# Performance work log

Hardware: AMD Instinct MI355X
Metric: run time of the kernel (lower is better)

Reference implementation:

```python
import jax, jax.numpy as jnp
import numpy as np


def setup_inputs() -> dict:
    key = jax.random.key(0)
    tensor = jax.random.normal(key, (4096, 3072), dtype=jnp.float32)
    return {"tensor": tensor}


def reference(tensor) -> jnp.ndarray:
    # Original: full_products[i,j] = mean_d((x_i * x_j)^2), zero diagonal, sum.
    # Identity: mean_d((x_i*x_j)^2) = (1/D) * sum_d (x_i^2)_d (x_j^2)_d = (Y Y^T / D)[i,j] with Y = x^2.
    B = tensor.shape[0]
    Y = jnp.square(tensor.reshape(B, -1))  # [B, D]
    D = Y.shape[1]
    G = jnp.matmul(Y, Y.T) / D  # [B, B] Gram of squared features
    # sum over off-diagonal entries == total sum minus trace
    return jnp.sum(G) - jnp.trace(G)
```

## Files before the change

kernel.cpp:

```cpp
#include <hip/hip_runtime.h>


typedef float f4 __attribute__((ext_vector_type(4)));

#define NROWS 4096
#define NCOLS 3072
#define NC4     768
#define GBX     24
#define NCHUNK  64
#define NBLK1   (GBX * NCHUNK)
#define TPB     256
#define DINV (1.0 / (double)NCOLS)

#define WS_CS_OFF  0
#define WS_COL_OFF 128
#define WS_Q_OFF   (WS_COL_OFF + NCHUNK * NCOLS * 4)
#define WS_CNT_OFF (WS_Q_OFF + NBLK1 * 4)

__global__ __launch_bounds__(TPB) void k1_colsq(const float* __restrict__ x,
                                                float* __restrict__ col_part,
                                                float* __restrict__ q_part,
                                                unsigned int* __restrict__ counter) {
    const int t    = threadIdx.x;
    const int tc   = t & 31;
    const int rsub = t >> 5;
    const int c4   = blockIdx.x * 32 + tc;
    const int r0   = blockIdx.y * 64 + rsub * 8;
    const f4* __restrict__ xv = (const f4*)x;

    if (t == 0 && blockIdx.x == 0 && blockIdx.y == 0) *counter = 0u;

    f4 s = (f4)(0.f);
    float q = 0.f;
    #pragma unroll
    for (int i = 0; i < 8; ++i) {
        f4 v = __builtin_nontemporal_load(&xv[(size_t)(r0 + i) * NC4 + c4]);
        f4 sq = v * v;
        s += sq;
        q = fmaf(sq.x, sq.x, q); q = fmaf(sq.y, sq.y, q);
        q = fmaf(sq.z, sq.z, q); q = fmaf(sq.w, sq.w, q);
    }

    __shared__ f4    part[7][32];
    __shared__ float qs[4];
    if (rsub) part[rsub - 1][tc] = s;
    #pragma unroll
    for (int off = 32; off; off >>= 1) q += __shfl_down(q, off);
    if ((t & 63) == 0) qs[t >> 6] = q;
    __syncthreads();

    if (rsub == 0) {
        f4 p = ((part[0][tc] + part[1][tc]) + (part[2][tc] + part[3][tc]))
             + ((part[4][tc] + part[5][tc]) + (part[6][tc] + s));
        ((f4*)col_part)[(size_t)blockIdx.y * NC4 + c4] = p;
    }
    if (t == 0)
        q_part[blockIdx.y * GBX + blockIdx.x] = (qs[0] + qs[1]) + (qs[2] + qs[3]);
}

__global__ __launch_bounds__(TPB) void k2_finish(const float* __restrict__ col_part,
                                                 const float* __restrict__ q_part,
                                                 double* __restrict__ cs_part,
                                                 unsigned int* __restrict__ counter,
                                                 float* __restrict__ out) {
    const int t = threadIdx.x;
    const int b = blockIdx.x;
    const int tc = t & 63, rsub = t >> 6;
    __shared__ f4 part[3][64];
    __shared__ double dsh[4];
    double partial = 0.0;

    if (b < 12) {
        const f4* __restrict__ cp4 = (const f4*)col_part;
        const int c4 = b * 64 + tc;
        f4 s = (f4)(0.f);
        #pragma unroll
        for (int i = 0; i < 16; ++i)
            s += cp4[(size_t)(rsub * 16 + i) * NC4 + c4];
        if (rsub) part[rsub - 1][tc] = s;
        __syncthreads();
        if (rsub == 0) {
            f4 p0 = part[0][tc], p1 = part[1][tc], p2 = part[2][tc];
            double cx = ((double)s.x + (double)p0.x) + ((double)p1.x + (double)p2.x);
            double cy = ((double)s.y + (double)p0.y) + ((double)p1.y + (double)p2.y);
            double cz = ((double)s.z + (double)p0.z) + ((double)p1.z + (double)p2.z);
            double cw = ((double)s.w + (double)p0.w) + ((double)p1.w + (double)p2.w);
            partial = (cx * cx + cy * cy) + (cz * cz + cw * cw);
            #pragma unroll
            for (int off = 32; off; off >>= 1) partial += __shfl_down(partial, off);
        }
    } else {
        double qd = 0.0;
        #pragma unroll
        for (int i = 0; i < 6; ++i) qd += (double)q_part[t + i * TPB];
        #pragma unroll
        for (int off = 32; off; off >>= 1) qd += __shfl_down(qd, off);
        if ((t & 63) == 0) dsh[rsub] = qd;
        __syncthreads();
        if (t == 0) partial = (dsh[0] + dsh[1]) + (dsh[2] + dsh[3]);
    }

    if (t == 0) {
        __hip_atomic_store(&cs_part[b], partial, __ATOMIC_RELEASE, __HIP_MEMORY_SCOPE_AGENT);
        unsigned int old = __hip_atomic_fetch_add(counter, 1u, __ATOMIC_ACQ_REL,
                                                  __HIP_MEMORY_SCOPE_AGENT);
        if (old == 12u) {
            double acc = 0.0;
            #pragma unroll
            for (int i = 0; i < 12; ++i)
                acc += __hip_atomic_load(&cs_part[i], __ATOMIC_ACQUIRE,
                                         __HIP_MEMORY_SCOPE_AGENT);
            acc -= __hip_atomic_load(&cs_part[12], __ATOMIC_ACQUIRE,
                                     __HIP_MEMORY_SCOPE_AGENT);
            out[0] = (float)(acc * DINV);
        }
    }
}

extern "C" void kernel_launch(void* const* d_in, const int* in_sizes, int n_in,
                              void* d_out, int out_size, void* d_ws, size_t ws_size,
                              hipStream_t stream) {
    const float* x = (const float*)d_in[0];
    float* out = (float*)d_out;
    char* ws = (char*)d_ws;
    double* cs_part  = (double*)(ws + WS_CS_OFF);
    float*  col_part = (float*)(ws + WS_COL_OFF);
    float*  q_part   = (float*)(ws + WS_Q_OFF);
    unsigned int* counter = (unsigned int*)(ws + WS_CNT_OFF);

    k1_colsq<<<dim3(GBX, NCHUNK), TPB, 0, stream>>>(x, col_part, q_part, counter);
    k2_finish<<<13, TPB, 0, stream>>>(col_part, q_part, cs_part, counter, out);
}
```

Measured before the change: 17.24 us.

## Restructure column-square reduction into full-row blocks with larger second-stage partials

The first kernel now runs 256 blocks of 768 threads, each covering 16 full rows, and writes its column partial sums straight out with no shared-memory combine. The second kernel then reduces 256 partial rows instead of 64, spread over 24 stripes plus one block for the squared-norm term. This removes the in-block LDS reduction in stage one and uses contiguous full-row reads. In exchange the intermediate buffer grows fourfold (about 3 MB) and stage two has to read more data.

```diff
diff --git a/kernel.cpp b/kernel.cpp
--- a/kernel.cpp
+++ b/kernel.cpp
@@ -6,96 +6,89 @@
 #define NROWS 4096
 #define NCOLS 3072
 #define NC4     768
-#define GBX     24
-#define NCHUNK  64
-#define NBLK1   (GBX * NCHUNK)
-#define TPB     256
+#define TPB1    768
+#define RPB     16
+#define NBLK1   (NROWS / RPB)
+#define NSTRIPE 24
+#define TPB2    256
 #define DINV (1.0 / (double)NCOLS)
 
 #define WS_CS_OFF  0
-#define WS_COL_OFF 128
-#define WS_Q_OFF   (WS_COL_OFF + NCHUNK * NCOLS * 4)
+#define WS_COL_OFF 256
+#define WS_Q_OFF   (WS_COL_OFF + NBLK1 * NCOLS * 4)
 #define WS_CNT_OFF (WS_Q_OFF + NBLK1 * 4)
 
-__global__ __launch_bounds__(TPB) void k1_colsq(const float* __restrict__ x,
-                                                float* __restrict__ col_part,
-                                                float* __restrict__ q_part,
-                                                unsigned int* __restrict__ counter) {
-    const int t    = threadIdx.x;
-    const int tc   = t & 31;
-    const int rsub = t >> 5;
-    const int c4   = blockIdx.x * 32 + tc;
-    const int r0   = blockIdx.y * 64 + rsub * 8;
+__global__ __launch_bounds__(TPB1) void k1_colsq(const float* __restrict__ x,
+                                                 float* __restrict__ col_part,
+                                                 float* __restrict__ q_part,
+                                                 unsigned int* __restrict__ counter) {
+    const int t = threadIdx.x;
+    const int b = blockIdx.x;
     const f4* __restrict__ xv = (const f4*)x;
+    const size_t base = (size_t)b * RPB * NC4 + t;
 
-    if (t == 0 && blockIdx.x == 0 && blockIdx.y == 0) *counter = 0u;
+    if (t == 0 && b == 0) *counter = 0u;
 
     f4 s = (f4)(0.f);
     float q = 0.f;
     #pragma unroll
-    for (int i = 0; i < 8; ++i) {
-        f4 v = __builtin_nontemporal_load(&xv[(size_t)(r0 + i) * NC4 + c4]);
+    for (int r = 0; r < RPB; ++r) {
+        f4 v = __builtin_nontemporal_load(&xv[base + (size_t)r * NC4]);
         f4 sq = v * v;
         s += sq;
         q = fmaf(sq.x, sq.x, q); q = fmaf(sq.y, sq.y, q);
         q = fmaf(sq.z, sq.z, q); q = fmaf(sq.w, sq.w, q);
     }
+    ((f4*)col_part)[(size_t)b * NC4 + t] = s;
 
-    __shared__ f4    part[7][32];
-    __shared__ float qs[4];
-    if (rsub) part[rsub - 1][tc] = s;
     #pragma unroll
     for (int off = 32; off; off >>= 1) q += __shfl_down(q, off);
+    __shared__ float qs[12];
     if ((t & 63) == 0) qs[t >> 6] = q;
     __syncthreads();
-
-    if (rsub == 0) {
-        f4 p = ((part[0][tc] + part[1][tc]) + (part[2][tc] + part[3][tc]))
-             + ((part[4][tc] + part[5][tc]) + (part[6][tc] + s));
-        ((f4*)col_part)[(size_t)blockIdx.y * NC4 + c4] = p;
+    if (t == 0) {
+        float qq = ((qs[0] + qs[1]) + (qs[2] + qs[3]))
+                 + ((qs[4] + qs[5]) + (qs[6] + qs[7]))
+                 + ((qs[8] + qs[9]) + (qs[10] + qs[11]));
+        q_part[b] = qq;
     }
-    if (t == 0)
-        q_part[blockIdx.y * GBX + blockIdx.x] = (qs[0] + qs[1]) + (qs[2] + qs[3]);
 }
 
-__global__ __launch_bounds__(TPB) void k2_finish(const float* __restrict__ col_part,
-                                                 const float* __restrict__ q_part,
-                                                 double* __restrict__ cs_part,
-                                                 unsigned int* __restrict__ counter,
-                                                 float* __restrict__ out) {
+__global__ __launch_bounds__(TPB2) void k2_finish(const float* __restrict__ col_part,
+                                                  const float* __restrict__ q_part,
+                                                  double* __restrict__ cs_part,
+                                                  unsigned int* __restrict__ counter,
+                                                  float* __restrict__ out) {
     const int t = threadIdx.x;
     const int b = blockIdx.x;
-    const int tc = t & 63, rsub = t >> 6;
-    __shared__ f4 part[3][64];
+    const int tc = t & 31, rsub = t >> 5;
+    __shared__ f4 part[7][32];
     __shared__ double dsh[4];
     double partial = 0.0;
 
-    if (b < 12) {
+    if (b < NSTRIPE) {
         const f4* __restrict__ cp4 = (const f4*)col_part;
-        const int c4 = b * 64 + tc;
+        const int c4 = b * 32 + tc;
         f4 s = (f4)(0.f);
         #pragma unroll
-        for (int i = 0; i < 16; ++i)
-            s += cp4[(size_t)(rsub * 16 + i) * NC4 + c4];
+        for (int i = 0; i < 32; ++i)
+            s += cp4[(size_t)(rsub * 32 + i) * NC4 + c4];
         if (rsub) part[rsub - 1][tc] = s;
         __syncthreads();
         if (rsub == 0) {
-            f4 p0 = part[0][tc], p1 = part[1][tc], p2 = part[2][tc];
-            double cx = ((double)s.x + (double)p0.x) + ((double)p1.x + (double)p2.x);
-            double cy = ((double)s.y + (double)p0.y) + ((double)p1.y + (double)p2.y);
-            double cz = ((double)s.z + (double)p0.z) + ((double)p1.z + (double)p2.z);
-            double cw = ((double)s.w + (double)p0.w) + ((double)p1.w + (double)p2.w);
+            f4 tot = ((s + part[0][tc]) + (part[1][tc] + part[2][tc]))
+                   + ((part[3][tc] + part[4][tc]) + (part[5][tc] + part[6][tc]));
+            double cx = (double)tot.x, cy = (double)tot.y;
+            double cz = (double)tot.z, cw = (double)tot.w;
             partial = (cx * cx + cy * cy) + (cz * cz + cw * cw);
             #pragma unroll
-            for (int off = 32; off; off >>= 1) partial += __shfl_down(partial, off);
+            for (int off = 16; off; off >>= 1) partial += __shfl_down(partial, off);
         }
     } else {
-        double qd = 0.0;
-        #pragma unroll
-        for (int i = 0; i < 6; ++i) qd += (double)q_part[t + i * TPB];
+        double qd = (double)q_part[t];
         #pragma unroll
         for (int off = 32; off; off >>= 1) qd += __shfl_down(qd, off);
-        if ((t & 63) == 0) dsh[rsub] = qd;
+        if ((t & 63) == 0) dsh[t >> 6] = qd;
         __syncthreads();
         if (t == 0) partial = (dsh[0] + dsh[1]) + (dsh[2] + dsh[3]);
     }
@@ -104,13 +97,13 @@
         __hip_atomic_store(&cs_part[b], partial, __ATOMIC_RELEASE, __HIP_MEMORY_SCOPE_AGENT);
         unsigned int old = __hip_atomic_fetch_add(counter, 1u, __ATOMIC_ACQ_REL,
                                                   __HIP_MEMORY_SCOPE_AGENT);
-        if (old == 12u) {
+        if (old == NSTRIPE) {
             double acc = 0.0;
             #pragma unroll
-            for (int i = 0; i < 12; ++i)
+            for (int i = 0; i < NSTRIPE; ++i)
                 acc += __hip_atomic_load(&cs_part[i], __ATOMIC_ACQUIRE,
                                          __HIP_MEMORY_SCOPE_AGENT);
-            acc -= __hip_atomic_load(&cs_part[12], __ATOMIC_ACQUIRE,
+            acc -= __hip_atomic_load(&cs_part[NSTRIPE], __ATOMIC_ACQUIRE,
                                      __HIP_MEMORY_SCOPE_AGENT);
             out[0] = (float)(acc * DINV);
         }
@@ -128,6 +121,6 @@
     float*  q_part   = (float*)(ws + WS_Q_OFF);
     unsigned int* counter = (unsigned int*)(ws + WS_CNT_OFF);
 
-    k1_colsq<<<dim3(GBX, NCHUNK), TPB, 0, stream>>>(x, col_part, q_part, counter);
-    k2_finish<<<13, TPB, 0, stream>>>(col_part, q_part, cs_part, counter, out);
+    k1_colsq<<<NBLK1, TPB1, 0, stream>>>(x, col_part, q_part, counter);
+    k2_finish<<<NSTRIPE + 1, TPB2, 0, stream>>>(col_part, q_part, cs_part, counter, out);
 }
```

After: 20.68 us. 19.9% more time.

## Fuse column reduction and finish into one kernel with float atomics and last-block tail

Applied to the files above, without the earlier changes.

Replaces the two-kernel scheme (per-chunk column partials, then a finishing kernel) with a single kernel. Each block atomically adds its column sums into one shared array of 3072 floats, and the last block to arrive, found with a counter, computes the sum of squares and subtracts the diagonal term. A memset clears the accumulators before the launch. This removes the partial-sum round trip and one kernel launch, but adds a memset operation, contention on float atomics (64 blocks per cell), and summation order that is no longer deterministic.

```diff
diff --git a/kernel.cpp b/kernel.cpp
--- a/kernel.cpp
+++ b/kernel.cpp
@@ -12,23 +12,24 @@
 #define TPB     256
 #define DINV (1.0 / (double)NCOLS)
 
-#define WS_CS_OFF  0
-#define WS_COL_OFF 128
-#define WS_Q_OFF   (WS_COL_OFF + NCHUNK * NCOLS * 4)
-#define WS_CNT_OFF (WS_Q_OFF + NBLK1 * 4)
+#define WS_CELLS_OFF  0
+#define WS_CNT_OFF    (NCOLS * 4)
+#define WS_ZERO_BYTES (NCOLS * 4 + 4)
+#define WS_Q_OFF      (NCOLS * 4 + 128)
 
-__global__ __launch_bounds__(TPB) void k1_colsq(const float* __restrict__ x,
-                                                float* __restrict__ col_part,
-                                                float* __restrict__ q_part,
-                                                unsigned int* __restrict__ counter) {
+__global__ __launch_bounds__(TPB) void fused_orthreg(
+        const float* __restrict__ x,
+        float* __restrict__ cells,
+        float* __restrict__ q_part,
+        unsigned int* __restrict__ counter,
+        float* __restrict__ out) {
     const int t    = threadIdx.x;
     const int tc   = t & 31;
     const int rsub = t >> 5;
     const int c4   = blockIdx.x * 32 + tc;
     const int r0   = blockIdx.y * 64 + rsub * 8;
+    const int bid  = blockIdx.y * GBX + blockIdx.x;
     const f4* __restrict__ xv = (const f4*)x;
-
-    if (t == 0 && blockIdx.x == 0 && blockIdx.y == 0) *counter = 0u;
 
     f4 s = (f4)(0.f);
     float q = 0.f;
@@ -43,6 +44,7 @@
 
     __shared__ f4    part[7][32];
     __shared__ float qs[4];
+    __shared__ int   lastflag;
     if (rsub) part[rsub - 1][tc] = s;
     #pragma unroll
     for (int off = 32; off; off >>= 1) q += __shfl_down(q, off);
@@ -52,69 +54,43 @@
     if (rsub == 0) {
         f4 p = ((part[0][tc] + part[1][tc]) + (part[2][tc] + part[3][tc]))
              + ((part[4][tc] + part[5][tc]) + (part[6][tc] + s));
-        ((f4*)col_part)[(size_t)blockIdx.y * NC4 + c4] = p;
-    }
-    if (t == 0)
-        q_part[blockIdx.y * GBX + blockIdx.x] = (qs[0] + qs[1]) + (qs[2] + qs[3]);
-}
-
-__global__ __launch_bounds__(TPB) void k2_finish(const float* __restrict__ col_part,
-                                                 const float* __restrict__ q_part,
-                                                 double* __restrict__ cs_part,
-                                                 unsigned int* __restrict__ counter,
-                                                 float* __restrict__ out) {
-    const int t = threadIdx.x;
-    const int b = blockIdx.x;
-    const int tc = t & 63, rsub = t >> 6;
-    __shared__ f4 part[3][64];
-    __shared__ double dsh[4];
-    double partial = 0.0;
-
-    if (b < 12) {
-        const f4* __restrict__ cp4 = (const f4*)col_part;
-        const int c4 = b * 64 + tc;
-        f4 s = (f4)(0.f);
-        #pragma unroll
-        for (int i = 0; i < 16; ++i)
-            s += cp4[(size_t)(rsub * 16 + i) * NC4 + c4];
-        if (rsub) part[rsub - 1][tc] = s;
-        __syncthreads();
-        if (rsub == 0) {
-            f4 p0 = part[0][tc], p1 = part[1][tc], p2 = part[2][tc];
-            double cx = ((double)s.x + (double)p0.x) + ((double)p1.x + (double)p2.x);
-            double cy = ((double)s.y + (double)p0.y) + ((double)p1.y + (double)p2.y);
-            double cz = ((double)s.z + (double)p0.z) + ((double)p1.z + (double)p2.z);
-            double cw = ((double)s.w + (double)p0.w) + ((double)p1.w + (double)p2.w);
-            partial = (cx * cx + cy * cy) + (cz * cz + cw * cw);
-            #pragma unroll
-            for (int off = 32; off; off >>= 1) partial += __shfl_down(partial, off);
-        }
-    } else {
-        double qd = 0.0;
-        #pragma unroll
-        for (int i = 0; i < 6; ++i) qd += (double)q_part[t + i * TPB];
-        #pragma unroll
-        for (int off = 32; off; off >>= 1) qd += __shfl_down(qd, off);
-        if ((t & 63) == 0) dsh[rsub] = qd;
-        __syncthreads();
-        if (t == 0) partial = (dsh[0] + dsh[1]) + (dsh[2] + dsh[3]);
-    }
-
-    if (t == 0) {
-        __hip_atomic_store(&cs_part[b], partial, __ATOMIC_RELEASE, __HIP_MEMORY_SCOPE_AGENT);
-        unsigned int old = __hip_atomic_fetch_add(counter, 1u, __ATOMIC_ACQ_REL,
-                                                  __HIP_MEMORY_SCOPE_AGENT);
-        if (old == 12u) {
-            double acc = 0.0;
-            #pragma unroll
-            for (int i = 0; i < 12; ++i)
-                acc += __hip_atomic_load(&cs_part[i], __ATOMIC_ACQUIRE,
-                                         __HIP_MEMORY_SCOPE_AGENT);
-            acc -= __hip_atomic_load(&cs_part[12], __ATOMIC_ACQUIRE,
-                                     __HIP_MEMORY_SCOPE_AGENT);
-            out[0] = (float)(acc * DINV);
+        __hip_atomic_fetch_add(&cells[c4 * 4 + 0], p.x, __ATOMIC_RELAXED, __HIP_MEMORY_SCOPE_AGENT);
+        __hip_atomic_fetch_add(&cells[c4 * 4 + 1], p.y, __ATOMIC_RELAXED, __HIP_MEMORY_SCOPE_AGENT);
+        __hip_atomic_fetch_add(&cells[c4 * 4 + 2], p.z, __ATOMIC_RELAXED, __HIP_MEMORY_SCOPE_AGENT);
+        __hip_atomic_fetch_add(&cells[c4 * 4 + 3], p.w, __ATOMIC_RELAXED, __HIP_MEMORY_SCOPE_AGENT);
+        if (t == 0) {
+            float qq = (qs[0] + qs[1]) + (qs[2] + qs[3]);
+            __hip_atomic_store(&q_part[bid], qq, __ATOMIC_RELAXED, __HIP_MEMORY_SCOPE_AGENT);
+            asm volatile("s_waitcnt vmcnt(0)" ::: "memory");
+            unsigned int old = __hip_atomic_fetch_add(counter, 1u, __ATOMIC_RELAXED,
+                                                      __HIP_MEMORY_SCOPE_AGENT);
+            lastflag = (old == NBLK1 - 1);
         }
     }
+    __syncthreads();
+    if (!lastflag) return;
+
+    double acc = 0.0;
+    #pragma unroll
+    for (int i = 0; i < NCOLS / TPB; ++i) {
+        float cv = __hip_atomic_load(&cells[t + i * TPB], __ATOMIC_RELAXED,
+                                     __HIP_MEMORY_SCOPE_AGENT);
+        double cd = (double)cv;
+        acc += cd * cd;
+    }
+    double qa = 0.0;
+    #pragma unroll
+    for (int i = 0; i < NBLK1 / TPB; ++i) {
+        qa += (double)__hip_atomic_load(&q_part[t + i * TPB], __ATOMIC_RELAXED,
+                                        __HIP_MEMORY_SCOPE_AGENT);
+    }
+    acc -= qa;
+    #pragma unroll
+    for (int off = 32; off; off >>= 1) acc += __shfl_down(acc, off);
+    __shared__ double dd[4];
+    if ((t & 63) == 0) dd[t >> 6] = acc;
+    __syncthreads();
+    if (t == 0) out[0] = (float)(((dd[0] + dd[1]) + (dd[2] + dd[3])) * DINV);
 }
 
 extern "C" void kernel_launch(void* const* d_in, const int* in_sizes, int n_in,
@@ -123,11 +99,10 @@
     const float* x = (const float*)d_in[0];
     float* out = (float*)d_out;
     char* ws = (char*)d_ws;
-    double* cs_part  = (double*)(ws + WS_CS_OFF);
-    float*  col_part = (float*)(ws + WS_COL_OFF);
-    float*  q_part   = (float*)(ws + WS_Q_OFF);
+    float* cells  = (float*)(ws + WS_CELLS_OFF);
+    float* q_part = (float*)(ws + WS_Q_OFF);
     unsigned int* counter = (unsigned int*)(ws + WS_CNT_OFF);
 
-    k1_colsq<<<dim3(GBX, NCHUNK), TPB, 0, stream>>>(x, col_part, q_part, counter);
-    k2_finish<<<13, TPB, 0, stream>>>(col_part, q_part, cs_part, counter, out);
+    (void)hipMemsetAsync(ws, 0, WS_ZERO_BYTES, stream);
+    fused_orthreg<<<dim3(GBX, NCHUNK), TPB, 0, stream>>>(x, cells, q_part, counter, out);
 }
```

Result: slower. 34.19 us (+98.3%).
